# Optimization experiments

Measured on AMD Instinct MI355X. Metric: run time of the kernel, lower is better.

Reference implementation:

```python
import jax, jax.numpy as jnp
import numpy as np

B, I, O = 32768, 512, 512
EPS = 1e-5


def setup_inputs() -> dict:
    key = jax.random.key(0)
    ks = jax.random.split(key, 4)
    return {
        "input": jax.random.normal(ks[0], (B, I), dtype=jnp.float32),
        "h": jax.random.normal(ks[1], (B, O), dtype=jnp.float32),
        "c": jax.random.normal(ks[2], (B, O), dtype=jnp.float32),
        "W": jax.random.normal(ks[3], (4 * O, I + O), dtype=jnp.float32) * (1.0 / np.sqrt(I + O)),
        "gamma": jnp.ones((4, O), dtype=jnp.float32),
        "beta": jnp.zeros((4, O), dtype=jnp.float32),
    }


def reference(input, h, c, W, gamma, beta):
    # fused input projection: [B, I+O] @ [I+O, 4O] -> [B, 4, O]
    z = jnp.einsum("bi,gi->bg", jnp.concatenate([input, h], axis=-1), W)
    z = z.reshape(z.shape[0], 4, O)
    # LayerNorm over the trailing [4, O] dims jointly (torch LayerNorm([x, o_size]))
    mean = jnp.mean(z, axis=(-2, -1), keepdims=True)
    var = jnp.var(z, axis=(-2, -1), keepdims=True)
    zn = (z - mean) * jax.lax.rsqrt(var + EPS) * gamma + beta
    f_gate = jax.nn.sigmoid(zn[:, 0])
    i_gate = jax.nn.sigmoid(zn[:, 1])
    o_gate = jax.nn.sigmoid(zn[:, 2])
    # GELU (torch default = exact erf); dropout is identity in eval mode
    h_state = jax.nn.gelu(zn[:, 3], approximate=False)
    cell = f_gate * c + i_gate * h_state
    output = o_gate * cell
    return (output, cell)
```

## Files before the change

### kernel.cpp

```cpp
#include <hip/hip_runtime.h>
#include <hip/hip_bf16.h>
#include <cstdint>
#include <cstddef>

#define BDIM 32768
#define IDIM 512
#define ODIM 512
#define KDIM 1024
#define NDIM 2048

typedef __attribute__((ext_vector_type(8))) __bf16 bf16x8;
typedef __attribute__((ext_vector_type(4))) float f32x4;
typedef __attribute__((ext_vector_type(8))) unsigned short u16x8;

__device__ __forceinline__ unsigned short f2bf(float x) {
  union { float f; uint32_t u; } v; v.f = x;
  uint32_t r = v.u + 0x7FFFu + ((v.u >> 16) & 1u);
  return (unsigned short)(r >> 16);
}

__device__ __forceinline__ float bf2f(unsigned short s) {
  union { uint32_t u; float f; } v; v.u = ((uint32_t)s) << 16;
  return v.f;
}


__global__ __launch_bounds__(256) void pack_a_kernel(const float* __restrict__ in,
                                                     const float* __restrict__ h,
                                                     unsigned short* __restrict__ A) {
  size_t t = (size_t)blockIdx.x * 256 + threadIdx.x;
  size_t e = t * 8;
  size_t b = e >> 10;
  int col = (int)(e & 1023);
  const float* src = (col < IDIM) ? (in + b * IDIM + col)
                                  : (h + b * ODIM + (col - IDIM));
  float4 v0 = ((const float4*)src)[0];
  float4 v1 = ((const float4*)src)[1];
  u16x8 r;
  r[0] = f2bf(v0.x); r[1] = f2bf(v0.y); r[2] = f2bf(v0.z); r[3] = f2bf(v0.w);
  r[4] = f2bf(v1.x); r[5] = f2bf(v1.y); r[6] = f2bf(v1.z); r[7] = f2bf(v1.w);
  *(u16x8*)(A + e) = r;
}

__global__ __launch_bounds__(256) void pack_w_kernel(const float* __restrict__ Wsrc,
                                                     unsigned short* __restrict__ Wb) {
  size_t t = (size_t)blockIdx.x * 256 + threadIdx.x;
  size_t e = t * 8;
  float4 v0 = ((const float4*)(Wsrc + e))[0];
  float4 v1 = ((const float4*)(Wsrc + e))[1];
  u16x8 r;
  r[0] = f2bf(v0.x); r[1] = f2bf(v0.y); r[2] = f2bf(v0.z); r[3] = f2bf(v0.w);
  r[4] = f2bf(v1.x); r[5] = f2bf(v1.y); r[6] = f2bf(v1.z); r[7] = f2bf(v1.w);
  *(u16x8*)(Wb + e) = r;
}


#define TM 128
#define TN 128
#define TK 64

__global__ __launch_bounds__(256) void gemm_kernel(const unsigned short* __restrict__ A,
                                                   const unsigned short* __restrict__ Bt,
                                                   unsigned short* __restrict__ Cz) {
  __shared__ unsigned short As[TM][TK];
  __shared__ unsigned short Bs[TN][TK];
  const int tid = threadIdx.x;
  const int wave = tid >> 6;
  const int lane = tid & 63;
  const int m0 = blockIdx.x * TM;
  const int n0 = blockIdx.y * TN;
  const int wm = (wave >> 1) * 64;
  const int wn = (wave & 1) * 64;

  f32x4 acc[4][4] = {};

  const int r_in_chunk = lane >> 3;
  const int kc = (lane & 7) * 8;

  for (int kt = 0; kt < KDIM / TK; ++kt) {
    const int k0 = kt * TK;
    __syncthreads();
#pragma unroll
    for (int i = 0; i < 4; ++i) {
      const int chunk = i * 4 + wave;
      const int row = chunk * 8 + r_in_chunk;
      __builtin_amdgcn_global_load_lds(
          (const __attribute__((address_space(1))) void*)(A + (size_t)(m0 + row) * KDIM + k0 + kc),
          (__attribute__((address_space(3))) void*)((char*)(&As[0][0]) + chunk * 1024),
          16, 0, 0);
      __builtin_amdgcn_global_load_lds(
          (const __attribute__((address_space(1))) void*)(Bt + (size_t)(n0 + row) * KDIM + k0 + kc),
          (__attribute__((address_space(3))) void*)((char*)(&Bs[0][0]) + chunk * 1024),
          16, 0, 0);
    }
    __syncthreads();
#pragma unroll
    for (int kk = 0; kk < TK; kk += 32) {
      bf16x8 af[4], bfr[4];
#pragma unroll
      for (int mi = 0; mi < 4; ++mi)
        af[mi] = *(const bf16x8*)&As[wm + mi * 16 + (lane & 15)][kk + (lane >> 4) * 8];
#pragma unroll
      for (int ni = 0; ni < 4; ++ni)
        bfr[ni] = *(const bf16x8*)&Bs[wn + ni * 16 + (lane & 15)][kk + (lane >> 4) * 8];
#pragma unroll
      for (int mi = 0; mi < 4; ++mi)
#pragma unroll
        for (int ni = 0; ni < 4; ++ni)
          acc[mi][ni] = __builtin_amdgcn_mfma_f32_16x16x32_bf16(af[mi], bfr[ni], acc[mi][ni], 0, 0, 0);
    }
  }

#pragma unroll
  for (int mi = 0; mi < 4; ++mi) {
#pragma unroll
    for (int ni = 0; ni < 4; ++ni) {
#pragma unroll
      for (int r = 0; r < 4; ++r) {
        const int row = m0 + wm + mi * 16 + (lane >> 4) * 4 + r;
        const int col = n0 + wn + ni * 16 + (lane & 15);
        Cz[(size_t)row * NDIM + col] = f2bf(acc[mi][ni][r]);
      }
    }
  }
}


__global__ __launch_bounds__(256) void ln_gate_kernel(const unsigned short* __restrict__ z,
                                                      const float* __restrict__ c,
                                                      const float* __restrict__ gamma,
                                                      const float* __restrict__ beta,
                                                      float* __restrict__ out) {
  __shared__ float rowbuf[4][NDIM];
  const int wave = threadIdx.x >> 6;
  const int lane = threadIdx.x & 63;
  const int row = blockIdx.x * 4 + wave;
  const unsigned short* zr = z + (size_t)row * NDIM;

  float s = 0.f, ss = 0.f;
#pragma unroll
  for (int j = 0; j < 4; ++j) {
    const int chunk = j * 64 + lane;
    u16x8 v = *(const u16x8*)(zr + chunk * 8);
    float f[8];
#pragma unroll
    for (int i2 = 0; i2 < 8; ++i2) {
      f[i2] = bf2f(v[i2]);
      s += f[i2];
      ss += f[i2] * f[i2];
    }
    float4* dst = (float4*)&rowbuf[wave][chunk * 8];
    dst[0] = make_float4(f[0], f[1], f[2], f[3]);
    dst[1] = make_float4(f[4], f[5], f[6], f[7]);
  }
#pragma unroll
  for (int off = 32; off > 0; off >>= 1) {
    s += __shfl_xor(s, off, 64);
    ss += __shfl_xor(ss, off, 64);
  }
  const float mean = s * (1.f / (float)NDIM);
  const float var = ss * (1.f / (float)NDIM) - mean * mean;
  const float inv = rsqrtf(var + 1e-5f);

  float* out_o = out + (size_t)row * ODIM;
  float* out_c = out + (size_t)BDIM * ODIM + (size_t)row * ODIM;
  const float* crow = c + (size_t)row * ODIM;

#pragma unroll
  for (int j = 0; j < 8; ++j) {
    const int o = j * 64 + lane;
    float zn[4];
#pragma unroll
    for (int g = 0; g < 4; ++g) {
      float v = (rowbuf[wave][g * ODIM + o] - mean) * inv;
      zn[g] = v * gamma[g * ODIM + o] + beta[g * ODIM + o];
    }
    const float fg = 1.f / (1.f + expf(-zn[0]));
    const float ig = 1.f / (1.f + expf(-zn[1]));
    const float og = 1.f / (1.f + expf(-zn[2]));
    const float x = zn[3];
    const float hs = 0.5f * x * (1.f + erff(x * 0.70710678118654752f));
    const float cc = fg * crow[o] + ig * hs;
    out_c[o] = cc;
    out_o[o] = og * cc;
  }
}


extern "C" void kernel_launch(void* const* d_in, const int* in_sizes, int n_in,
                              void* d_out, int out_size, void* d_ws, size_t ws_size,
                              hipStream_t stream) {
  const float* input = (const float*)d_in[0];
  const float* h     = (const float*)d_in[1];
  const float* c     = (const float*)d_in[2];
  const float* W     = (const float*)d_in[3];
  const float* gamma = (const float*)d_in[4];
  const float* beta  = (const float*)d_in[5];

  unsigned short* A  = (unsigned short*)d_ws;
  unsigned short* Wb = A + (size_t)BDIM * KDIM;
  unsigned short* z  = Wb + (size_t)NDIM * KDIM;
  float* out = (float*)d_out;

  pack_a_kernel<<<(BDIM * KDIM / 8) / 256, 256, 0, stream>>>(input, h, A);
  pack_w_kernel<<<(NDIM * KDIM / 8) / 256, 256, 0, stream>>>(W, Wb);
  dim3 ggrid(BDIM / TM, NDIM / TN);
  gemm_kernel<<<ggrid, 256, 0, stream>>>(A, Wb, z);
  ln_gate_kernel<<<BDIM / 4, 256, 0, stream>>>(z, c, gamma, beta, out);
}
```

Before: 301.3 us.

## Rewrite GEMM as 256x256 tile, 4-stage LDS pipeline with swizzled layout

Replaces the 128x128 single-buffered GEMM with a 512-thread kernel that computes 256x256 output tiles over a four-buffer ring of 32-row K slices in 128KB of dynamic LDS. Async global-to-LDS loads run three stages ahead, gated by explicit vmcnt waits and barriers. MFMA bursts are raised in priority, LDS columns are XOR-swizzled to avoid bank conflicts, and block IDs are remapped for L2 locality. This targets load latency and low MFMA utilisation in the old loop. The cost is high register pressure from 32 accumulators per lane and fragile manual synchronisation.

Result: faster. 271.3 us (-10.0%).

```diff
diff --git a/kernel.cpp b/kernel.cpp
--- a/kernel.cpp
+++ b/kernel.cpp
@@ -55,70 +55,164 @@
 }
 
 
-#define TM 128
-#define TN 128
-#define TK 64
-
-__global__ __launch_bounds__(256) void gemm_kernel(const unsigned short* __restrict__ A,
-                                                   const unsigned short* __restrict__ Bt,
-                                                   unsigned short* __restrict__ Cz) {
-  __shared__ unsigned short As[TM][TK];
-  __shared__ unsigned short Bs[TN][TK];
+#define BUFSZ 32768
+#define ABYTES 16384
+
+#define BAR() do { asm volatile("" ::: "memory"); __builtin_amdgcn_s_barrier(); asm volatile("" ::: "memory"); } while (0)
+#define VMW(n) asm volatile("s_waitcnt vmcnt(" #n ")" ::: "memory")
+
+__device__ __forceinline__ void gll16(const unsigned short* src, char* ldsdst) {
+  __builtin_amdgcn_global_load_lds(
+      (const __attribute__((address_space(1))) void*)src,
+      (__attribute__((address_space(3))) void*)ldsdst, 16, 0, 0);
+}
+
+template<int BUF, int VM, bool STG, int TO>
+__device__ __forceinline__ void tile_body(char* smem,
+                                          const unsigned short* sA0, const unsigned short* sA1,
+                                          const unsigned short* sB0, const unsigned short* sB1,
+                                          int wave1024, int aoff, int boff,
+                                          f32x4 (&acc)[8][4]) {
+  char* const Ab = smem + BUF * BUFSZ;
+  char* const Bb = Ab + ABYTES;
+  constexpr int DB = ((BUF + 3) & 3) * BUFSZ;
+
+  if (VM == 8)      VMW(8);
+  else if (VM == 4) VMW(4);
+  else              VMW(0);
+  BAR();
+
+  bf16x8 x0 = *(const bf16x8*)(Ab + aoff + 0 * 1024);
+  bf16x8 x1 = *(const bf16x8*)(Ab + aoff + 1 * 1024);
+  bf16x8 x2 = *(const bf16x8*)(Ab + aoff + 2 * 1024);
+  bf16x8 x3 = *(const bf16x8*)(Ab + aoff + 3 * 1024);
+  bf16x8 b0 = *(const bf16x8*)(Bb + boff + 0 * 1024);
+  bf16x8 b1 = *(const bf16x8*)(Bb + boff + 1 * 1024);
+  bf16x8 b2 = *(const bf16x8*)(Bb + boff + 2 * 1024);
+  bf16x8 b3 = *(const bf16x8*)(Bb + boff + 3 * 1024);
+  if (STG) {
+    gll16(sA0 + TO * 32, smem + DB + wave1024);
+    gll16(sB0 + TO * 32, smem + DB + ABYTES + wave1024);
+  }
+  BAR();
+  __builtin_amdgcn_sched_barrier(0);
+  __builtin_amdgcn_s_setprio(1);
+  acc[0][0] = __builtin_amdgcn_mfma_f32_16x16x32_bf16(x0, b0, acc[0][0], 0, 0, 0);
+  acc[0][1] = __builtin_amdgcn_mfma_f32_16x16x32_bf16(x0, b1, acc[0][1], 0, 0, 0);
+  acc[0][2] = __builtin_amdgcn_mfma_f32_16x16x32_bf16(x0, b2, acc[0][2], 0, 0, 0);
+  acc[0][3] = __builtin_amdgcn_mfma_f32_16x16x32_bf16(x0, b3, acc[0][3], 0, 0, 0);
+  acc[1][0] = __builtin_amdgcn_mfma_f32_16x16x32_bf16(x1, b0, acc[1][0], 0, 0, 0);
+  acc[1][1] = __builtin_amdgcn_mfma_f32_16x16x32_bf16(x1, b1, acc[1][1], 0, 0, 0);
+  acc[1][2] = __builtin_amdgcn_mfma_f32_16x16x32_bf16(x1, b2, acc[1][2], 0, 0, 0);
+  acc[1][3] = __builtin_amdgcn_mfma_f32_16x16x32_bf16(x1, b3, acc[1][3], 0, 0, 0);
+  acc[2][0] = __builtin_amdgcn_mfma_f32_16x16x32_bf16(x2, b0, acc[2][0], 0, 0, 0);
+  acc[2][1] = __builtin_amdgcn_mfma_f32_16x16x32_bf16(x2, b1, acc[2][1], 0, 0, 0);
+  acc[2][2] = __builtin_amdgcn_mfma_f32_16x16x32_bf16(x2, b2, acc[2][2], 0, 0, 0);
+  acc[2][3] = __builtin_amdgcn_mfma_f32_16x16x32_bf16(x2, b3, acc[2][3], 0, 0, 0);
+  acc[3][0] = __builtin_amdgcn_mfma_f32_16x16x32_bf16(x3, b0, acc[3][0], 0, 0, 0);
+  acc[3][1] = __builtin_amdgcn_mfma_f32_16x16x32_bf16(x3, b1, acc[3][1], 0, 0, 0);
+  acc[3][2] = __builtin_amdgcn_mfma_f32_16x16x32_bf16(x3, b2, acc[3][2], 0, 0, 0);
+  acc[3][3] = __builtin_amdgcn_mfma_f32_16x16x32_bf16(x3, b3, acc[3][3], 0, 0, 0);
+  __builtin_amdgcn_s_setprio(0);
+  __builtin_amdgcn_sched_barrier(0);
+  BAR();
+
+  x0 = *(const bf16x8*)(Ab + aoff + 4 * 1024);
+  x1 = *(const bf16x8*)(Ab + aoff + 5 * 1024);
+  x2 = *(const bf16x8*)(Ab + aoff + 6 * 1024);
+  x3 = *(const bf16x8*)(Ab + aoff + 7 * 1024);
+  if (STG) {
+    gll16(sA1 + TO * 32, smem + DB + 8192 + wave1024);
+    gll16(sB1 + TO * 32, smem + DB + ABYTES + 8192 + wave1024);
+  }
+  BAR();
+  __builtin_amdgcn_sched_barrier(0);
+  __builtin_amdgcn_s_setprio(1);
+  acc[4][0] = __builtin_amdgcn_mfma_f32_16x16x32_bf16(x0, b0, acc[4][0], 0, 0, 0);
+  acc[4][1] = __builtin_amdgcn_mfma_f32_16x16x32_bf16(x0, b1, acc[4][1], 0, 0, 0);
+  acc[4][2] = __builtin_amdgcn_mfma_f32_16x16x32_bf16(x0, b2, acc[4][2], 0, 0, 0);
+  acc[4][3] = __builtin_amdgcn_mfma_f32_16x16x32_bf16(x0, b3, acc[4][3], 0, 0, 0);
+  acc[5][0] = __builtin_amdgcn_mfma_f32_16x16x32_bf16(x1, b0, acc[5][0], 0, 0, 0);
+  acc[5][1] = __builtin_amdgcn_mfma_f32_16x16x32_bf16(x1, b1, acc[5][1], 0, 0, 0);
+  acc[5][2] = __builtin_amdgcn_mfma_f32_16x16x32_bf16(x1, b2, acc[5][2], 0, 0, 0);
+  acc[5][3] = __builtin_amdgcn_mfma_f32_16x16x32_bf16(x1, b3, acc[5][3], 0, 0, 0);
+  acc[6][0] = __builtin_amdgcn_mfma_f32_16x16x32_bf16(x2, b0, acc[6][0], 0, 0, 0);
+  acc[6][1] = __builtin_amdgcn_mfma_f32_16x16x32_bf16(x2, b1, acc[6][1], 0, 0, 0);
+  acc[6][2] = __builtin_amdgcn_mfma_f32_16x16x32_bf16(x2, b2, acc[6][2], 0, 0, 0);
+  acc[6][3] = __builtin_amdgcn_mfma_f32_16x16x32_bf16(x2, b3, acc[6][3], 0, 0, 0);
+  acc[7][0] = __builtin_amdgcn_mfma_f32_16x16x32_bf16(x3, b0, acc[7][0], 0, 0, 0);
+  acc[7][1] = __builtin_amdgcn_mfma_f32_16x16x32_bf16(x3, b1, acc[7][1], 0, 0, 0);
+  acc[7][2] = __builtin_amdgcn_mfma_f32_16x16x32_bf16(x3, b2, acc[7][2], 0, 0, 0);
+  acc[7][3] = __builtin_amdgcn_mfma_f32_16x16x32_bf16(x3, b3, acc[7][3], 0, 0, 0);
+  __builtin_amdgcn_s_setprio(0);
+  __builtin_amdgcn_sched_barrier(0);
+}
+
+__global__ __launch_bounds__(512, 2) void gemm_kernel(const unsigned short* __restrict__ A,
+                                                      const unsigned short* __restrict__ Bt,
+                                                      unsigned short* __restrict__ Cz) {
+  extern __shared__ char smem[];
   const int tid = threadIdx.x;
   const int wave = tid >> 6;
   const int lane = tid & 63;
-  const int m0 = blockIdx.x * TM;
-  const int n0 = blockIdx.y * TN;
-  const int wm = (wave >> 1) * 64;
-  const int wn = (wave & 1) * 64;
-
-  f32x4 acc[4][4] = {};
-
-  const int r_in_chunk = lane >> 3;
-  const int kc = (lane & 7) * 8;
-
-  for (int kt = 0; kt < KDIM / TK; ++kt) {
-    const int k0 = kt * TK;
-    __syncthreads();
-#pragma unroll
-    for (int i = 0; i < 4; ++i) {
-      const int chunk = i * 4 + wave;
-      const int row = chunk * 8 + r_in_chunk;
-      __builtin_amdgcn_global_load_lds(
-          (const __attribute__((address_space(1))) void*)(A + (size_t)(m0 + row) * KDIM + k0 + kc),
-          (__attribute__((address_space(3))) void*)((char*)(&As[0][0]) + chunk * 1024),
-          16, 0, 0);
-      __builtin_amdgcn_global_load_lds(
-          (const __attribute__((address_space(1))) void*)(Bt + (size_t)(n0 + row) * KDIM + k0 + kc),
-          (__attribute__((address_space(3))) void*)((char*)(&Bs[0][0]) + chunk * 1024),
-          16, 0, 0);
-    }
-    __syncthreads();
-#pragma unroll
-    for (int kk = 0; kk < TK; kk += 32) {
-      bf16x8 af[4], bfr[4];
-#pragma unroll
-      for (int mi = 0; mi < 4; ++mi)
-        af[mi] = *(const bf16x8*)&As[wm + mi * 16 + (lane & 15)][kk + (lane >> 4) * 8];
-#pragma unroll
-      for (int ni = 0; ni < 4; ++ni)
-        bfr[ni] = *(const bf16x8*)&Bs[wn + ni * 16 + (lane & 15)][kk + (lane >> 4) * 8];
-#pragma unroll
-      for (int mi = 0; mi < 4; ++mi)
-#pragma unroll
-        for (int ni = 0; ni < 4; ++ni)
-          acc[mi][ni] = __builtin_amdgcn_mfma_f32_16x16x32_bf16(af[mi], bfr[ni], acc[mi][ni], 0, 0, 0);
-    }
-  }
-
-#pragma unroll
-  for (int mi = 0; mi < 4; ++mi) {
+
+  const int bid = blockIdx.x;
+  const int swz = (bid & 7) * 128 + (bid >> 3);
+  const int m0 = (swz >> 3) * 256;
+  const int n0 = (swz & 7) * 256;
+
+  const int wm = (wave >> 2) * 128;
+  const int wn = (wave & 3) * 64;
+  const int lrow = lane & 15;
+  const int cswz16 = (((lane >> 4) ^ (lrow >> 2)) & 3) * 16;
+  const int aoff = (wm + lrow) * 64 + cswz16;
+  const int boff = (wn + lrow) * 64 + cswz16;
+  const int wave1024 = wave * 1024;
+
+  const int r0 = tid >> 2;
+  const int r1 = r0 + 128;
+  const int c0 = (tid & 3) ^ ((r0 >> 2) & 3);
+  const int c1 = (tid & 3) ^ ((r1 >> 2) & 3);
+  const unsigned short* sA0 = A  + (size_t)(m0 + r0) * KDIM + c0 * 8;
+  const unsigned short* sA1 = A  + (size_t)(m0 + r1) * KDIM + c1 * 8;
+  const unsigned short* sB0 = Bt + (size_t)(n0 + r0) * KDIM + c0 * 8;
+  const unsigned short* sB1 = Bt + (size_t)(n0 + r1) * KDIM + c1 * 8;
+
+  f32x4 acc[8][4] = {};
+
+  gll16(sA0,      smem + 0 * BUFSZ + wave1024);
+  gll16(sB0,      smem + 0 * BUFSZ + ABYTES + wave1024);
+  gll16(sA1,      smem + 0 * BUFSZ + 8192 + wave1024);
+  gll16(sB1,      smem + 0 * BUFSZ + ABYTES + 8192 + wave1024);
+  gll16(sA0 + 32, smem + 1 * BUFSZ + wave1024);
+  gll16(sB0 + 32, smem + 1 * BUFSZ + ABYTES + wave1024);
+  gll16(sA1 + 32, smem + 1 * BUFSZ + 8192 + wave1024);
+  gll16(sB1 + 32, smem + 1 * BUFSZ + ABYTES + 8192 + wave1024);
+  gll16(sA0 + 64, smem + 2 * BUFSZ + wave1024);
+  gll16(sB0 + 64, smem + 2 * BUFSZ + ABYTES + wave1024);
+  gll16(sA1 + 64, smem + 2 * BUFSZ + 8192 + wave1024);
+  gll16(sB1 + 64, smem + 2 * BUFSZ + ABYTES + 8192 + wave1024);
+
+  for (int t4 = 0; t4 < 28; t4 += 4) {
+    tile_body<0, 8, true, 3>(smem, sA0, sA1, sB0, sB1, wave1024, aoff, boff, acc);
+    tile_body<1, 8, true, 4>(smem, sA0, sA1, sB0, sB1, wave1024, aoff, boff, acc);
+    tile_body<2, 8, true, 5>(smem, sA0, sA1, sB0, sB1, wave1024, aoff, boff, acc);
+    tile_body<3, 8, true, 6>(smem, sA0, sA1, sB0, sB1, wave1024, aoff, boff, acc);
+    sA0 += 128; sA1 += 128; sB0 += 128; sB1 += 128;
+  }
+  tile_body<0, 8, true,  3>(smem, sA0, sA1, sB0, sB1, wave1024, aoff, boff, acc);
+  tile_body<1, 8, false, 0>(smem, sA0, sA1, sB0, sB1, wave1024, aoff, boff, acc);
+  tile_body<2, 4, false, 0>(smem, sA0, sA1, sB0, sB1, wave1024, aoff, boff, acc);
+  tile_body<3, 0, false, 0>(smem, sA0, sA1, sB0, sB1, wave1024, aoff, boff, acc);
+
+#pragma unroll
+  for (int mi = 0; mi < 8; ++mi) {
 #pragma unroll
     for (int ni = 0; ni < 4; ++ni) {
 #pragma unroll
       for (int r = 0; r < 4; ++r) {
         const int row = m0 + wm + mi * 16 + (lane >> 4) * 4 + r;
-        const int col = n0 + wn + ni * 16 + (lane & 15);
+        const int col = n0 + wn + ni * 16 + lrow;
         Cz[(size_t)row * NDIM + col] = f2bf(acc[mi][ni][r]);
       }
     }
@@ -202,9 +296,11 @@
   unsigned short* z  = Wb + (size_t)NDIM * KDIM;
   float* out = (float*)d_out;
 
+  hipFuncSetAttribute((const void*)gemm_kernel,
+                      hipFuncAttributeMaxDynamicSharedMemorySize, 131072);
+
   pack_a_kernel<<<(BDIM * KDIM / 8) / 256, 256, 0, stream>>>(input, h, A);
   pack_w_kernel<<<(NDIM * KDIM / 8) / 256, 256, 0, stream>>>(W, Wb);
-  dim3 ggrid(BDIM / TM, NDIM / TN);
-  gemm_kernel<<<ggrid, 256, 0, stream>>>(A, Wb, z);
+  gemm_kernel<<<dim3((BDIM / 256) * (NDIM / 256)), 512, 131072, stream>>>(A, Wb, z);
   ln_gate_kernel<<<BDIM / 4, 256, 0, stream>>>(z, c, gamma, beta, out);
 }
```

## Rewrite GEMM as 256x256 double-buffered pipelined kernel with 8 waves

Applied to the files above, without the earlier changes.

Replaces the 128x128 single-buffered GEMM with a 256x256-tile kernel using 512 threads, 128 KB of dynamic LDS split into two buffers, and an interleaved schedule. Global-to-LDS loads for the next K tile are issued between MFMA phases, with explicit vmcnt/lgkmcnt waits, barriers and s_setprio. A grouped block-index swizzle is added for L2 locality. The aim is to hide memory latency and raise MFMA utilisation. The cost is higher register and LDS pressure and fragile hand-written synchronisation.

Result: faster. 284.0 us (-5.7%).

```diff
diff --git a/kernel.cpp b/kernel.cpp
--- a/kernel.cpp
+++ b/kernel.cpp
@@ -55,70 +55,137 @@
 }
 
 
-#define TM 128
-#define TN 128
-#define TK 64
-
-__global__ __launch_bounds__(256) void gemm_kernel(const unsigned short* __restrict__ A,
-                                                   const unsigned short* __restrict__ Bt,
-                                                   unsigned short* __restrict__ Cz) {
-  __shared__ unsigned short As[TM][TK];
-  __shared__ unsigned short Bs[TN][TK];
+#define GB 65536
+
+#define BAR() do { asm volatile("" ::: "memory"); __builtin_amdgcn_s_barrier(); asm volatile("" ::: "memory"); } while (0)
+#define VMW(n) asm volatile("s_waitcnt vmcnt(" #n ")" ::: "memory")
+#define LGKM0() do { asm volatile("s_waitcnt lgkmcnt(0)" ::: "memory"); __builtin_amdgcn_sched_barrier(0); } while (0)
+
+__device__ __forceinline__ void gll16(const unsigned short* src, char* ldsdst) {
+  __builtin_amdgcn_global_load_lds(
+      (const __attribute__((address_space(1))) void*)src,
+      (__attribute__((address_space(3))) void*)ldsdst, 16, 0, 0);
+}
+
+__device__ __forceinline__ void mf16(const bf16x8 (&a)[4], const bf16x8 (&q)[4],
+                                     f32x4 (&acc)[8][4], int mb) {
+#pragma unroll
+  for (int i = 0; i < 4; ++i)
+#pragma unroll
+    for (int j = 0; j < 4; ++j)
+      acc[mb + i][j] = __builtin_amdgcn_mfma_f32_16x16x32_bf16(a[i], q[j], acc[mb + i][j], 0, 0, 0);
+}
+
+template<int BUF, bool STG, bool FINAL>
+__device__ __forceinline__ void ktile(char* aR, char* bR, char* stA, char* stB,
+                                      const unsigned short* pA0, const unsigned short* pA1,
+                                      const unsigned short* pB0, const unsigned short* pB1,
+                                      int stOff, f32x4 (&acc)[8][4]) {
+  bf16x8 af[4], qf[4];
+#pragma unroll
+  for (int i = 0; i < 4; ++i) af[i] = *(const bf16x8*)(aR + i * 1024);
+#pragma unroll
+  for (int j = 0; j < 4; ++j) qf[j] = *(const bf16x8*)(bR + j * 1024);
+  if (STG) { gll16(pA0, stA + stOff); gll16(pA1, stA + 8192 + stOff); }
+  BAR(); LGKM0();
+  __builtin_amdgcn_s_setprio(1);
+  mf16(af, qf, acc, 0);
+  __builtin_amdgcn_s_setprio(0);
+  __builtin_amdgcn_sched_barrier(0);
+  BAR();
+#pragma unroll
+  for (int i = 0; i < 4; ++i) af[i] = *(const bf16x8*)(aR + (4 + i) * 1024);
+  if (STG) { gll16(pB0, stB + stOff); gll16(pB1, stB + 8192 + stOff); }
+  BAR(); LGKM0();
+  __builtin_amdgcn_s_setprio(1);
+  mf16(af, qf, acc, 4);
+  __builtin_amdgcn_s_setprio(0);
+  __builtin_amdgcn_sched_barrier(0);
+  if (FINAL) VMW(0); else VMW(4);
+  BAR();
+#pragma unroll
+  for (int i = 0; i < 4; ++i) af[i] = *(const bf16x8*)(aR + 16384 + i * 1024);
+#pragma unroll
+  for (int j = 0; j < 4; ++j) qf[j] = *(const bf16x8*)(bR + 16384 + j * 1024);
+  if (STG) { gll16(pA0 + 32, stA + 16384 + stOff); gll16(pA1 + 32, stA + 24576 + stOff); }
+  BAR(); LGKM0();
+  __builtin_amdgcn_s_setprio(1);
+  mf16(af, qf, acc, 0);
+  __builtin_amdgcn_s_setprio(0);
+  __builtin_amdgcn_sched_barrier(0);
+  BAR();
+#pragma unroll
+  for (int i = 0; i < 4; ++i) af[i] = *(const bf16x8*)(aR + 16384 + (4 + i) * 1024);
+  if (STG) { gll16(pB0 + 32, stB + 16384 + stOff); gll16(pB1 + 32, stB + 24576 + stOff); }
+  BAR(); LGKM0();
+  __builtin_amdgcn_s_setprio(1);
+  mf16(af, qf, acc, 4);
+  __builtin_amdgcn_s_setprio(0);
+  __builtin_amdgcn_sched_barrier(0);
+  if (!FINAL) VMW(4);
+  BAR();
+}
+
+__global__ __launch_bounds__(512, 2) void gemm_kernel(const unsigned short* __restrict__ A,
+                                                      const unsigned short* __restrict__ Bt,
+                                                      unsigned short* __restrict__ Cz) {
+  extern __shared__ char smem[];
   const int tid = threadIdx.x;
-  const int wave = tid >> 6;
+  const int w = tid >> 6;
   const int lane = tid & 63;
-  const int m0 = blockIdx.x * TM;
-  const int n0 = blockIdx.y * TN;
-  const int wm = (wave >> 1) * 64;
-  const int wn = (wave & 1) * 64;
-
-  f32x4 acc[4][4] = {};
-
-  const int r_in_chunk = lane >> 3;
-  const int kc = (lane & 7) * 8;
-
-  for (int kt = 0; kt < KDIM / TK; ++kt) {
-    const int k0 = kt * TK;
-    __syncthreads();
-#pragma unroll
-    for (int i = 0; i < 4; ++i) {
-      const int chunk = i * 4 + wave;
-      const int row = chunk * 8 + r_in_chunk;
-      __builtin_amdgcn_global_load_lds(
-          (const __attribute__((address_space(1))) void*)(A + (size_t)(m0 + row) * KDIM + k0 + kc),
-          (__attribute__((address_space(3))) void*)((char*)(&As[0][0]) + chunk * 1024),
-          16, 0, 0);
-      __builtin_amdgcn_global_load_lds(
-          (const __attribute__((address_space(1))) void*)(Bt + (size_t)(n0 + row) * KDIM + k0 + kc),
-          (__attribute__((address_space(3))) void*)((char*)(&Bs[0][0]) + chunk * 1024),
-          16, 0, 0);
-    }
-    __syncthreads();
-#pragma unroll
-    for (int kk = 0; kk < TK; kk += 32) {
-      bf16x8 af[4], bfr[4];
-#pragma unroll
-      for (int mi = 0; mi < 4; ++mi)
-        af[mi] = *(const bf16x8*)&As[wm + mi * 16 + (lane & 15)][kk + (lane >> 4) * 8];
-#pragma unroll
-      for (int ni = 0; ni < 4; ++ni)
-        bfr[ni] = *(const bf16x8*)&Bs[wn + ni * 16 + (lane & 15)][kk + (lane >> 4) * 8];
-#pragma unroll
-      for (int mi = 0; mi < 4; ++mi)
-#pragma unroll
-        for (int ni = 0; ni < 4; ++ni)
-          acc[mi][ni] = __builtin_amdgcn_mfma_f32_16x16x32_bf16(af[mi], bfr[ni], acc[mi][ni], 0, 0, 0);
-    }
-  }
-
-#pragma unroll
-  for (int mi = 0; mi < 4; ++mi) {
+
+  const int bid = blockIdx.x;
+  const int swz = (bid & 7) * 128 + (bid >> 3);
+  const int m0 = (swz >> 3) * 256;
+  const int n0 = (swz & 7) * 256;
+
+  const int wm = (w >> 2) * 128;
+  const int wn = (w & 3) * 64;
+  const int lrow = lane & 15;
+  const int lk = (lane >> 4) * 8;
+
+  char* aR0 = smem + (w >> 2) * 8192 + lane * 16;
+  char* bR0 = smem + 32768 + (w & 3) * 4096 + lane * 16;
+  char* aR1 = aR0 + GB;
+  char* bR1 = bR0 + GB;
+  const int stOff = w * 1024 + lane * 16;
+
+  const unsigned short* pA0 = A  + (size_t)(m0 + w * 16       + lrow) * KDIM + lk;
+  const unsigned short* pA1 = A  + (size_t)(m0 + (8 + w) * 16 + lrow) * KDIM + lk;
+  const unsigned short* pB0 = Bt + (size_t)(n0 + w * 16       + lrow) * KDIM + lk;
+  const unsigned short* pB1 = Bt + (size_t)(n0 + (8 + w) * 16 + lrow) * KDIM + lk;
+
+  f32x4 acc[8][4] = {};
+
+  gll16(pA0,      smem + stOff);
+  gll16(pA1,      smem + 8192 + stOff);
+  gll16(pB0,      smem + 32768 + stOff);
+  gll16(pB1,      smem + 40960 + stOff);
+  gll16(pA0 + 32, smem + 16384 + stOff);
+  gll16(pA1 + 32, smem + 24576 + stOff);
+  gll16(pB0 + 32, smem + 49152 + stOff);
+  gll16(pB1 + 32, smem + 57344 + stOff);
+  VMW(4);
+  BAR();
+  pA0 += 64; pA1 += 64; pB0 += 64; pB1 += 64;
+
+  for (int tt = 0; tt < 7; ++tt) {
+    ktile<0, true, false>(aR0, bR0, smem + GB, smem + GB + 32768, pA0, pA1, pB0, pB1, stOff, acc);
+    pA0 += 64; pA1 += 64; pB0 += 64; pB1 += 64;
+    ktile<1, true, false>(aR1, bR1, smem, smem + 32768, pA0, pA1, pB0, pB1, stOff, acc);
+    pA0 += 64; pA1 += 64; pB0 += 64; pB1 += 64;
+  }
+  ktile<0, true, false>(aR0, bR0, smem + GB, smem + GB + 32768, pA0, pA1, pB0, pB1, stOff, acc);
+  ktile<1, false, true>(aR1, bR1, smem, smem + 32768, pA0, pA1, pB0, pB1, stOff, acc);
+
+#pragma unroll
+  for (int mi = 0; mi < 8; ++mi) {
 #pragma unroll
     for (int ni = 0; ni < 4; ++ni) {
 #pragma unroll
       for (int r = 0; r < 4; ++r) {
         const int row = m0 + wm + mi * 16 + (lane >> 4) * 4 + r;
-        const int col = n0 + wn + ni * 16 + (lane & 15);
+        const int col = n0 + wn + ni * 16 + lrow;
         Cz[(size_t)row * NDIM + col] = f2bf(acc[mi][ni][r]);
       }
     }
@@ -202,9 +269,11 @@
   unsigned short* z  = Wb + (size_t)NDIM * KDIM;
   float* out = (float*)d_out;
 
+  hipFuncSetAttribute((const void*)gemm_kernel,
+                      hipFuncAttributeMaxDynamicSharedMemorySize, 131072);
+
   pack_a_kernel<<<(BDIM * KDIM / 8) / 256, 256, 0, stream>>>(input, h, A);
   pack_w_kernel<<<(NDIM * KDIM / 8) / 256, 256, 0, stream>>>(W, Wb);
-  dim3 ggrid(BDIM / TM, NDIM / TN);
-  gemm_kernel<<<ggrid, 256, 0, stream>>>(A, Wb, z);
+  gemm_kernel<<<dim3((BDIM / 256) * (NDIM / 256)), 512, 131072, stream>>>(A, Wb, z);
   ln_gate_kernel<<<BDIM / 4, 256, 0, stream>>>(z, c, gamma, beta, out);
 }
```
